# Performance work log

Measured on AMD Instinct MI355X. Metric: run time of the kernel, lower is better.

## Reference

```python
import jax, jax.numpy as jnp
import numpy as np

NTOKEN = 32000
NINP = 512
NHIDLAST = 1024
N_EXPERTS = 10
N = 1024


def setup_inputs() -> dict:
    key = jax.random.key(0)
    ks = jax.random.split(key, 4)
    return {
        "output": jax.random.normal(ks[0], (N, NHIDLAST), dtype=jnp.float32),
        "W_latent": jax.random.normal(ks[1], (N_EXPERTS * NINP, NHIDLAST), dtype=jnp.float32) * 0.02,
        "b_latent": jnp.zeros((N_EXPERTS * NINP,), dtype=jnp.float32),
        "W_decoder": jax.random.normal(ks[2], (NTOKEN, NINP), dtype=jnp.float32) * 0.02,
        "b_decoder": jnp.zeros((NTOKEN,), dtype=jnp.float32),
        "W_reduce": jax.random.normal(ks[3], (N_EXPERTS, NHIDLAST), dtype=jnp.float32) * 0.02,
        "b_reduce": jnp.zeros((N_EXPERTS,), dtype=jnp.float32),
        "dropoutl": 0,
    }


def reference(output, W_latent, b_latent, W_decoder, b_decoder, W_reduce, b_reduce, dropoutl):
    n = output.shape[0]
    # latent projection + tanh; lockdrop with rate 0 is identity
    latent = jnp.tanh(output @ W_latent.T + b_latent)            # [N, E*ninp]
    logit = latent.reshape(n * N_EXPERTS, NINP) @ W_decoder.T + b_decoder  # [N*E, V]
    # stick-breaking Beta parameters
    a = jax.nn.softplus(output @ W_reduce.T + b_reduce) + 1e-8   # [N, E]
    b = jnp.sum(a, axis=1)                                       # [N]
    c = jnp.cumsum(a, axis=1)                                    # [N, E]
    d = jnp.abs(b[:, None] - c)                                  # remaining mass
    d = jnp.maximum(d, 1e-8)  # last column is exactly 0; avoid Beta(a,0) NaN
    sample = jax.random.beta(jax.random.key(42), a, d)           # reparameterized Beta
    # rem @ diag(ones, offset=1) shifts columns right by one; rem[:,0]=1
    rem = 1.0 - sample
    rem_shift = jnp.concatenate([jnp.ones((n, 1), dtype=rem.dtype), rem[:, :-1]], axis=1)
    remprod = jnp.cumprod(rem_shift, axis=1)
    pis = remprod * sample                                       # [N, E] mixture weights
    prob = jax.nn.softmax(logit.reshape(n, N_EXPERTS, NTOKEN), axis=-1)
    out = jnp.einsum('net,ne->nt', prob, pis)                    # [N, V]
    return out
```

## Files before the change

### kernel.cpp

```cpp
#include <hip/hip_runtime.h>
#include <cstdint>
#include <cstddef>

#pragma clang fp contract(off)

#define NTOK  32000
#define NINP  512
#define NHID  1024
#define NEXP  10
#define NROW  1024
#define NLAT  (NEXP*NINP)
#define MROWS (NROW*NEXP)

typedef __attribute__((ext_vector_type(4))) float f32x4;
typedef __attribute__((ext_vector_type(8))) short bf16x8;
typedef __attribute__((ext_vector_type(8))) unsigned short us16x8;

#define GLD16(g, l) __builtin_amdgcn_global_load_lds(                       \
    (const __attribute__((address_space(1))) void*)(g),                     \
    (__attribute__((address_space(3))) void*)(l), 16, 0, 0)

__device__ __forceinline__ unsigned short f2b(float x) {
    uint32_t u = __float_as_uint(x);
    uint32_t r = (u + 0x7fffu + ((u >> 16) & 1u)) >> 16;
    return (unsigned short)r;
}
__device__ __forceinline__ float b2f(unsigned short b) {
    return __uint_as_float(((uint32_t)b) << 16);
}

__device__ __forceinline__ uint32_t rotl32(uint32_t v, int r) {
    return (v << r) | (v >> (32 - r));
}

__device__ __forceinline__ void threefry(uint32_t k0, uint32_t k1,
                                         uint32_t x0, uint32_t x1,
                                         uint32_t& o0, uint32_t& o1) {
    uint32_t k2 = k0 ^ k1 ^ 0x1BD11BDAu;
    x0 += k0; x1 += k1;
#define TF_R(r) { x0 += x1; x1 = rotl32(x1, r); x1 ^= x0; }
    TF_R(13) TF_R(15) TF_R(26) TF_R(6)
    x0 += k1; x1 += k2 + 1u;
    TF_R(17) TF_R(29) TF_R(16) TF_R(24)
    x0 += k2; x1 += k0 + 2u;
    TF_R(13) TF_R(15) TF_R(26) TF_R(6)
    x0 += k0; x1 += k1 + 3u;
    TF_R(17) TF_R(29) TF_R(16) TF_R(24)
    x0 += k1; x1 += k2 + 4u;
    TF_R(13) TF_R(15) TF_R(26) TF_R(6)
    x0 += k2; x1 += k0 + 5u;
#undef TF_R
    o0 = x0; o1 = x1;
}

struct RKey { uint32_t a, b; };

__device__ __forceinline__ RKey kfold(RKey k, uint32_t i) {
    RKey r; threefry(k.a, k.b, 0u, i, r.a, r.b); return r;
}
__device__ __forceinline__ uint32_t kbits(RKey k) {
    uint32_t o0, o1; threefry(k.a, k.b, 0u, 0u, o0, o1); return o0 ^ o1;
}
__device__ __forceinline__ float u01(RKey k) {
    uint32_t b = (kbits(k) >> 9) | 0x3f800000u;
    return __uint_as_float(b) - 1.0f;
}
__device__ __forceinline__ float erfinv_xla(float x) {
    float xx = x * x;
    float w = -log1pf(-xx);
    float p;
    if (w < 5.0f) {
        float ww = w - 2.5f;
        p = 2.81022636e-08f;
        p = p * ww; p = p + 3.43273939e-07f;
        p = p * ww; p = p + -3.5233877e-06f;
        p = p * ww; p = p + -4.39150654e-06f;
        p = p * ww; p = p + 0.00021858087f;
        p = p * ww; p = p + -0.00125372503f;
        p = p * ww; p = p + -0.00417768164f;
        p = p * ww; p = p + 0.246640727f;
        p = p * ww; p = p + 1.50140941f;
    } else {
        float ww = sqrtf(w) - 3.0f;
        p = -0.000200214257f;
        p = p * ww; p = p + 0.000100950558f;
        p = p * ww; p = p + 0.00134934322f;
        p = p * ww; p = p + -0.00367342844f;
        p = p * ww; p = p + 0.00573950773f;
        p = p * ww; p = p + -0.0076224613f;
        p = p * ww; p = p + 0.00943887047f;
        p = p * ww; p = p + 1.00167406f;
        p = p * ww; p = p + 2.83297682f;
    }
    return p * x;
}
__device__ __forceinline__ float norm1(RKey k) {
    const float lo = -0.99999994f;
    float f = u01(k);
    float u = f * 2.0f;
    u = u + lo;
    u = fmaxf(lo, u);
    return 1.41421356f * erfinv_xla(u);
}

__device__ float gamma_log(RKey key, float alpha) {
    const float one_third = 0.33333334f;
    bool boost = (alpha >= 1.0f);
    float alpha_orig = alpha;
    if (!boost) alpha = alpha + 1.0f;
    float d = alpha - one_third;
    float c = one_third / sqrtf(d);

    RKey sub = kfold(key, 1u);
    key      = kfold(key, 0u);
    float log_boost = 0.0f;
    if (!boost) {
        float uB = u01(sub);
        log_boost = log1pf(-uB) * (1.0f / alpha_orig);
    }

    float X = 0.f, V = 1.f, U = 2.f;
    int guard = 0;
    do {
        RKey xk = kfold(key, 1u);
        RKey Uk = kfold(key, 2u);
        key     = kfold(key, 0u);
        float x = 0.f, v = -1.f;
        RKey kin = xk;
        int g2 = 0;
        do {
            RKey sk = kfold(kin, 1u);
            kin     = kfold(kin, 0u);
            x = norm1(sk);
            float cx = x * c;
            v = 1.0f + cx;
        } while (v <= 0.0f && ++g2 < 256);
        X = x * x;
        V = (v * v) * v;
        U = u01(Uk);
        float sq = 1.0f - 0.0331f * (X * X);
        if (U < sq) break;
        float bound = (X * 0.5f) + ((d - d * V) + d * logf(V));
        if (logf(U) < bound) break;
    } while (++guard < 256);

    float ls = logf(d) + logf(V);
    ls = ls + log_boost;
    return ls;
}

__global__ void k_a(const float* __restrict__ out_in,
                    const float* __restrict__ Wred,
                    const float* __restrict__ bred,
                    float* __restrict__ a_arr, float* __restrict__ dpar) {
    int n = blockIdx.x;
    int lane = threadIdx.x;
    __shared__ float zred[NEXP];
    const float* orow = out_in + (size_t)n * NHID;
    for (int e = 0; e < NEXP; ++e) {
        const float* wrow = Wred + (size_t)e * NHID;
        float s = 0.f;
        for (int k = lane; k < NHID; k += 64) s += orow[k] * wrow[k];
        for (int off = 32; off; off >>= 1) s += __shfl_xor(s, off);
        if (lane == 0) zred[e] = s + bred[e];
    }
    __syncthreads();
    if (lane == 0) {
        float a[NEXP];
        float b = 0.f;
        for (int e = 0; e < NEXP; ++e) {
            float z = zred[e];
            a[e] = fmaxf(z, 0.f) + log1pf(expf(-fabsf(z))) + 1e-8f;
        }
        for (int e = 0; e < NEXP; ++e) b += a[e];
        float cs = 0.f;
        for (int e = 0; e < NEXP; ++e) {
            cs += a[e];
            float dd = fmaxf(fabsf(b - cs), 1e-8f);
            a_arr[n * NEXP + e] = a[e];
            dpar [n * NEXP + e] = dd;
        }
    }
}

__global__ void k_sample(const float* __restrict__ a_arr,
                         const float* __restrict__ dpar,
                         float* __restrict__ sample) {
    int i = blockIdx.x * 256 + threadIdx.x;
    if (i >= MROWS) return;
    RKey root{0u, 42u};
    RKey ka = kfold(root, 0u);
    RKey kb = kfold(root, 1u);
    float lga = gamma_log(kfold(ka, (uint32_t)i), a_arr[i]);
    float lgb = gamma_log(kfold(kb, (uint32_t)i), dpar[i]);
    float lm = fmaxf(lga, lgb);
    float ea = expf(lga - lm), eb = expf(lgb - lm);
    sample[i] = ea / (ea + eb);
}

__global__ void k_pis(const float* __restrict__ sample, float* __restrict__ pis) {
    int n = blockIdx.x * blockDim.x + threadIdx.x;
    if (n >= NROW) return;
    float rp = 1.0f;
    for (int e = 0; e < NEXP; ++e) {
        float s = sample[n * NEXP + e];
        pis[n * NEXP + e] = rp * s;
        rp = rp * (1.0f - s);
    }
}

__global__ void k_w(const float* __restrict__ pis, const float* __restrict__ Z,
                    float* __restrict__ w, int r0, int cnt) {
    int i = blockIdx.x * 256 + threadIdx.x;
    if (i >= cnt) return;
    int r = r0 + i;
    w[r] = pis[r] / Z[r];
}

__global__ void k_cvt(const float* __restrict__ src, unsigned short* __restrict__ dst, int n) {
    int i = (blockIdx.x * 256 + threadIdx.x) * 8;
    if (i >= n) return;
    float4 v0 = *(const float4*)(src + i);
    float4 v1 = *(const float4*)(src + i + 4);
    us16x8 o;
    o[0] = f2b(v0.x); o[1] = f2b(v0.y); o[2] = f2b(v0.z); o[3] = f2b(v0.w);
    o[4] = f2b(v1.x); o[5] = f2b(v1.y); o[6] = f2b(v1.z); o[7] = f2b(v1.w);
    *(us16x8*)(dst + i) = o;
}

__device__ __forceinline__ void combine_span(const unsigned short* __restrict__ P,
                                             const float* __restrict__ pis,
                                             const float* __restrict__ Z,
                                             float* __restrict__ out,
                                             int n0, int items, int idx0, int stride) {
    for (int idx = idx0; idx < items; idx += stride) {
        int nl = idx / 4000;
        int c8 = (idx - nl * 4000) * 8;
        int n  = n0 + nl;
        float w[NEXP];
#pragma unroll
        for (int e = 0; e < NEXP; ++e)
            w[e] = pis[n * NEXP + e] / Z[n * NEXP + e];
        float s[8] = {0.f,0.f,0.f,0.f,0.f,0.f,0.f,0.f};
        const unsigned short* Pr = P + (size_t)nl * NEXP * NTOK + c8;
#pragma unroll
        for (int e = 0; e < NEXP; ++e) {
            us16x8 v = __builtin_nontemporal_load((const us16x8*)(Pr + (size_t)e * NTOK));
#pragma unroll
            for (int jj = 0; jj < 8; ++jj)
                s[jj] = s[jj] + w[e] * b2f(v[jj]);
        }
        float* orow = out + (size_t)n * NTOK + c8;
        f32x4 o0 = {s[0], s[1], s[2], s[3]};
        f32x4 o1 = {s[4], s[5], s[6], s[7]};
        __builtin_nontemporal_store(o0, (f32x4*)(orow));
        __builtin_nontemporal_store(o1, (f32x4*)(orow + 4));
    }
}

__global__ __launch_bounds__(256)
void k_fin(const unsigned short* __restrict__ P,
           const float* __restrict__ pis,
           const float* __restrict__ Z,
           float* __restrict__ out, int n0, int items) {
    combine_span(P, pis, Z, out, n0, items,
                 (int)(blockIdx.x * 256u + threadIdx.x),
                 (int)(gridDim.x * 256u));
}

__global__ __launch_bounds__(256)
void k_latm(const unsigned short* __restrict__ A,
            const unsigned short* __restrict__ B,
            const float* __restrict__ bias,
            unsigned short* __restrict__ dst) {
    __shared__ unsigned short Als[2][128 * 64];
    __shared__ unsigned short Bls[2][128 * 64];
    const int tid  = threadIdx.x;
    const int lane = tid & 63, wid = tid >> 6;
    const int wm = wid >> 1, wn = wid & 1;
    const uint32_t l = blockIdx.x;
    const int row0 = (int)(l & 7u) * 128;
    const int col0 = (int)(l >> 3) * 128;
    const int lrow8 = lane >> 3, lslot = lane & 7;

    const unsigned short* pA[4];
    const unsigned short* pB[4];
#pragma unroll
    for (int i = 0; i < 4; ++i) {
        int rA = wid * 32 + i * 8 + lrow8;
        pA[i] = A + (size_t)(row0 + rA) * NHID + ((lslot ^ (rA & 7)) << 3);
        int rB = wid * 32 + i * 8 + lrow8;
        pB[i] = B + (size_t)(col0 + rB) * NHID + ((lslot ^ (rB & 7)) << 3);
    }
    int offA[2][4], offB[2][4];
#pragma unroll
    for (int kh = 0; kh < 2; ++kh)
#pragma unroll
        for (int f = 0; f < 4; ++f) {
            int rA = wm * 64 + f * 16 + (lane & 15);
            offA[kh][f] = rA * 128 + ((((lane >> 4) * 16) + kh * 64) ^ ((rA & 7) << 4));
            int rB = wn * 64 + f * 16 + (lane & 15);
            offB[kh][f] = rB * 128 + ((((lane >> 4) * 16) + kh * 64) ^ ((rB & 7) << 4));
        }

    f32x4 acc[4][4];
#pragma unroll
    for (int mf = 0; mf < 4; ++mf)
#pragma unroll
        for (int nf = 0; nf < 4; ++nf) acc[mf][nf] = (f32x4)0.f;

#pragma unroll
    for (int i = 0; i < 4; ++i) {
        GLD16(pA[i], (char*)&Als[0][0] + (wid * 32 + i * 8) * 128); pA[i] += 64;
        GLD16(pB[i], (char*)&Bls[0][0] + (wid * 32 + i * 8) * 128); pB[i] += 64;
    }
    __syncthreads();

#pragma unroll
    for (int t = 0; t < 16; ++t) {
        const int cur = t & 1, nxt = cur ^ 1;
        if (t < 15) {
#pragma unroll
            for (int i = 0; i < 4; ++i) {
                GLD16(pA[i], (char*)&Als[nxt][0] + (wid * 32 + i * 8) * 128); pA[i] += 64;
                GLD16(pB[i], (char*)&Bls[nxt][0] + (wid * 32 + i * 8) * 128); pB[i] += 64;
            }
        }
        const char* Ab = (const char*)&Als[cur][0];
        const char* Bb = (const char*)&Bls[cur][0];
#pragma unroll
        for (int kh = 0; kh < 2; ++kh) {
            bf16x8 af[4], bfr[4];
#pragma unroll
            for (int f = 0; f < 4; ++f) {
                af[f]  = *(const bf16x8*)(Ab + offA[kh][f]);
                bfr[f] = *(const bf16x8*)(Bb + offB[kh][f]);
            }
#pragma unroll
            for (int mf = 0; mf < 4; ++mf)
#pragma unroll
                for (int nf = 0; nf < 4; ++nf)
                    acc[mf][nf] = __builtin_amdgcn_mfma_f32_16x16x32_bf16(
                        af[mf], bfr[nf], acc[mf][nf], 0, 0, 0);
        }
        __syncthreads();
    }

    const int q = lane >> 4, cl = lane & 15;
#pragma unroll
    for (int mf = 0; mf < 4; ++mf) {
#pragma unroll
        for (int nf = 0; nf < 4; ++nf) {
            int col = col0 + wn * 64 + nf * 16 + cl;
            float bc = bias[col];
#pragma unroll
            for (int j = 0; j < 4; ++j) {
                int r = row0 + wm * 64 + mf * 16 + q * 4 + j;
                dst[(size_t)r * NLAT + col] = f2b(tanhf(acc[mf][nf][j] + bc));
            }
        }
    }
}

template<int MODE>
__global__ __launch_bounds__(256)
void k_dec(const unsigned short* __restrict__ A,
           const unsigned short* __restrict__ B,
           const float* __restrict__ bias,
           const float* __restrict__ wmix,
           float* __restrict__ dst,
           unsigned short* __restrict__ Pst,
           int rb0, int nRB, int nGemm,
           const float* __restrict__ pis,
           const float* __restrict__ Zarr,
           float* __restrict__ outp,
           const unsigned short* __restrict__ Pprev,
           int n0prev, int itemsPrev) {
    if (MODE == 3 && (int)blockIdx.x >= nGemm) {
        const int cb = (int)blockIdx.x - nGemm;
        combine_span(Pprev, pis, Zarr, outp, n0prev, itemsPrev,
                     cb * 256 + (int)threadIdx.x,
                     ((int)gridDim.x - nGemm) * 256);
        return;
    }
    __shared__ unsigned short Als[2][160 * 64];
    __shared__ unsigned short Bls[2][128 * 64];
    const int tid  = threadIdx.x;
    const int lane = tid & 63, wid = tid >> 6;
    const int wm = wid >> 1, wn = wid & 1;
    const uint32_t l = blockIdx.x;
    int by_l, bx;
    if (nRB >= 8) {
        const int per = nRB >> 3;
        const uint32_t jb = l >> 3;
        by_l = (int)(l & 7u) * per + (int)(jb % (uint32_t)per);
        bx   = (int)(jb / (uint32_t)per);
    } else {
        by_l = (int)(l % (uint32_t)nRB);
        bx   = (int)(l / (uint32_t)nRB);
    }
    const int by   = rb0 + by_l;
    const int row0 = by * 160;
    const int rl0  = by_l * 160;
    const int col0 = bx * 128;
    const int lrow8 = lane >> 3, lslot = lane & 7;

    const unsigned short* pA[5];
    const unsigned short* pB[4];
#pragma unroll
    for (int i = 0; i < 5; ++i) {
        int rA = wid * 40 + i * 8 + lrow8;
        pA[i] = A + (size_t)(row0 + rA) * 512 + ((lslot ^ (rA & 7)) << 3);
    }
#pragma unroll
    for (int i = 0; i < 4; ++i) {
        int rB = wid * 32 + i * 8 + lrow8;
        pB[i] = B + (size_t)(col0 + rB) * 512 + ((lslot ^ (rB & 7)) << 3);
    }
    int offA[2][5], offB[2][4];
#pragma unroll
    for (int kh = 0; kh < 2; ++kh) {
#pragma unroll
        for (int mf = 0; mf < 5; ++mf) {
            int r = wm * 80 + mf * 16 + (lane & 15);
            offA[kh][mf] = r * 128 + ((((lane >> 4) * 16) + kh * 64) ^ ((r & 7) << 4));
        }
#pragma unroll
        for (int nf = 0; nf < 4; ++nf) {
            int r = wn * 64 + nf * 16 + (lane & 15);
            offB[kh][nf] = r * 128 + ((((lane >> 4) * 16) + kh * 64) ^ ((r & 7) << 4));
        }
    }

    f32x4 acc[5][4];
#pragma unroll
    for (int mf = 0; mf < 5; ++mf)
#pragma unroll
        for (int nf = 0; nf < 4; ++nf) acc[mf][nf] = (f32x4)0.f;

#pragma unroll
    for (int i = 0; i < 5; ++i) {
        GLD16(pA[i], (char*)&Als[0][0] + (wid * 40 + i * 8) * 128); pA[i] += 64;
    }
#pragma unroll
    for (int i = 0; i < 4; ++i) {
        GLD16(pB[i], (char*)&Bls[0][0] + (wid * 32 + i * 8) * 128); pB[i] += 64;
    }
    __syncthreads();

#pragma unroll
    for (int t = 0; t < 8; ++t) {
        const int cur = t & 1, nxt = cur ^ 1;
        if (t < 7) {
#pragma unroll
            for (int i = 0; i < 5; ++i) {
                GLD16(pA[i], (char*)&Als[nxt][0] + (wid * 40 + i * 8) * 128); pA[i] += 64;
            }
#pragma unroll
            for (int i = 0; i < 4; ++i) {
                GLD16(pB[i], (char*)&Bls[nxt][0] + (wid * 32 + i * 8) * 128); pB[i] += 64;
            }
        }
        const char* Ab = (const char*)&Als[cur][0];
        const char* Bb = (const char*)&Bls[cur][0];
#pragma unroll
        for (int kh = 0; kh < 2; ++kh) {
            bf16x8 af[5], bfr[4];
#pragma unroll
            for (int mf = 0; mf < 5; ++mf)
                af[mf] = *(const bf16x8*)(Ab + offA[kh][mf]);
#pragma unroll
            for (int nf = 0; nf < 4; ++nf)
                bfr[nf] = *(const bf16x8*)(Bb + offB[kh][nf]);
#pragma unroll
            for (int mf = 0; mf < 5; ++mf)
#pragma unroll
                for (int nf = 0; nf < 4; ++nf)
                    acc[mf][nf] = __builtin_amdgcn_mfma_f32_16x16x32_bf16(
                        af[mf], bfr[nf], acc[mf][nf], 0, 0, 0);
        }
        __syncthreads();
    }

    const int q = lane >> 4, cl = lane & 15;
    float bv[4];
#pragma unroll
    for (int nf = 0; nf < 4; ++nf) bv[nf] = bias[col0 + wn * 64 + nf * 16 + cl];

    if (MODE == 1 || MODE == 3) {
#pragma unroll
        for (int mf = 0; mf < 5; ++mf) {
#pragma unroll
            for (int jj = 0; jj < 4; ++jj) {
                const int rr = wm * 80 + mf * 16 + q * 4 + jj;
                float p0 = expf(acc[mf][0][jj] + bv[0]);
                float p1 = expf(acc[mf][1][jj] + bv[1]);
                float p2 = expf(acc[mf][2][jj] + bv[2]);
                float p3 = expf(acc[mf][3][jj] + bv[3]);
                float s = ((p0 + p1) + (p2 + p3));
                s += __shfl_xor(s, 1); s += __shfl_xor(s, 2);
                s += __shfl_xor(s, 4); s += __shfl_xor(s, 8);
                if (cl == 0) atomicAdd(&dst[row0 + rr], s);
                if (MODE == 3) {
                    unsigned short* prow =
                        Pst + (size_t)(rl0 + rr) * NTOK + col0 + wn * 64 + cl;
                    __builtin_nontemporal_store(f2b(p0), prow);
                    __builtin_nontemporal_store(f2b(p1), prow + 16);
                    __builtin_nontemporal_store(f2b(p2), prow + 32);
                    __builtin_nontemporal_store(f2b(p3), prow + 48);
                }
            }
        }
    } else {
        float wv[5][4];
#pragma unroll
        for (int mf = 0; mf < 5; ++mf)
#pragma unroll
            for (int jj = 0; jj < 4; ++jj)
                wv[mf][jj] = wmix[row0 + wm * 80 + mf * 16 + q * 4 + jj];
#pragma unroll
        for (int mf = 0; mf < 5; ++mf)
#pragma unroll
            for (int nf = 0; nf < 4; ++nf)
#pragma unroll
                for (int jj = 0; jj < 4; ++jj)
                    acc[mf][nf][jj] = wv[mf][jj] * expf(acc[mf][nf][jj] + bv[nf]);

        const int tok0 = by * 16 + wm * 8;
#pragma unroll
        for (int t = 0; t < 8; ++t) {
#pragma unroll
            for (int nf = 0; nf < 4; ++nf) {
                float s = 0.f;
#pragma unroll
                for (int i = 0; i < 10; ++i) {
                    const int rl = 10 * t + i;
                    const int mf = rl >> 4, qr = (rl >> 2) & 3, jj = rl & 3;
                    s += (q == qr) ? acc[mf][nf][jj] : 0.f;
                }
                s += __shfl_xor(s, 16);
                s += __shfl_xor(s, 32);
                if (q == 0)
                    dst[(size_t)(tok0 + t) * NTOK + col0 + wn * 64 + nf * 16 + cl] = s;
            }
        }
    }
}

extern "C" void kernel_launch(void* const* d_in, const int* in_sizes, int n_in,
                              void* d_out, int out_size, void* d_ws, size_t ws_size,
                              hipStream_t stream) {
    const float* output    = (const float*)d_in[0];
    const float* W_latent  = (const float*)d_in[1];
    const float* b_latent  = (const float*)d_in[2];
    const float* W_decoder = (const float*)d_in[3];
    const float* b_decoder = (const float*)d_in[4];
    const float* W_reduce  = (const float*)d_in[5];
    const float* b_reduce  = (const float*)d_in[6];
    float* out = (float*)d_out;

    char* wsb = (char*)d_ws;
    unsigned short* latb  = (unsigned short*)wsb;
    unsigned short* wdecb = (unsigned short*)(wsb + 10485760);
    float* a_arr  = (float*)(wsb + 10485760 + 32768000);
    float* dpar   = a_arr  + MROWS;
    float* sample = dpar   + MROWS;
    float* pis    = sample + MROWS;
    float* Z      = pis    + MROWS;
    float* wmix   = Z      + MROWS;
    unsigned short* Pbuf = (unsigned short*)(wmix + MROWS);
    const size_t BASE = 10485760ull + 32768000ull + 6ull * MROWS * 4ull;
    const size_t avail = (ws_size > BASE) ? (ws_size - BASE) : 0;

    int CRd = 0, CRs = 0;
    {
        const int cands[4] = {2560, 1280, 640, 320};
        for (int c = 0; c < 4; ++c)
            if (2ull * (size_t)cands[c] * NTOK * 2ull <= avail) { CRd = cands[c]; break; }
        if (CRd == 0) {
            const int cs[5] = {2560, 1280, 640, 320, 160};
            for (int c = 0; c < 5; ++c)
                if ((size_t)cs[c] * NTOK * 2ull <= avail) { CRs = cs[c]; break; }
        }
    }

    unsigned short* outb  = (unsigned short*)d_out;
    unsigned short* wlatb = (unsigned short*)((char*)d_out + 2097152);

    k_a<<<NROW, 64, 0, stream>>>(output, W_reduce, b_reduce, a_arr, dpar);
    k_sample<<<MROWS / 256, 256, 0, stream>>>(a_arr, dpar, sample);
    k_pis<<<(NROW + 255) / 256, 256, 0, stream>>>(sample, pis);

    k_cvt<<<(NTOK * NINP) / 2048, 256, 0, stream>>>(W_decoder, wdecb, NTOK * NINP);
    k_cvt<<<(NROW * NHID) / 2048, 256, 0, stream>>>(output, outb, NROW * NHID);
    k_cvt<<<(NLAT * NHID) / 2048, 256, 0, stream>>>(W_latent, wlatb, NLAT * NHID);

    k_latm<<<320, 256, 0, stream>>>(outb, wlatb, b_latent, latb);

    (void)hipMemsetAsync(Z, 0, MROWS * sizeof(float), stream);

    if (CRd > 0) {
        const int nRB = CRd / 160, nGemm = nRB * 250, nch = MROWS / CRd;
        const int items = (CRd / 10) * 4000;
        for (int ci = 0; ci < nch; ++ci) {
            unsigned short* Pcur  = Pbuf + (size_t)(ci & 1) * CRd * NTOK;
            unsigned short* Pprev = Pbuf + (size_t)((ci & 1) ^ 1) * CRd * NTOK;
            const int extra = (ci > 0) ? 1000 : 0;
            k_dec<3><<<nGemm + extra, 256, 0, stream>>>(
                latb, wdecb, b_decoder, nullptr, Z, Pcur, ci * nRB, nRB, nGemm,
                pis, Z, out, Pprev, (ci - 1) * (CRd / 10), items);
        }
        unsigned short* Plast = Pbuf + (size_t)((nch - 1) & 1) * CRd * NTOK;
        k_fin<<<items / 256, 256, 0, stream>>>(Plast, pis, Z, out,
                                               (nch - 1) * (CRd / 10), items);
    } else if (CRs > 0) {
        const int nRB = CRs / 160;
        const int items = (CRs / 10) * 4000;
        for (int r0 = 0; r0 < MROWS; r0 += CRs) {
            k_dec<3><<<nRB * 250, 256, 0, stream>>>(
                latb, wdecb, b_decoder, nullptr, Z, Pbuf, r0 / 160, nRB, 1 << 30,
                pis, Z, out, nullptr, 0, 0);
            k_fin<<<items / 256, 256, 0, stream>>>(Pbuf, pis, Z, out, r0 / 10, items);
        }
    } else {
        k_dec<1><<<16000, 256, 0, stream>>>(latb, wdecb, b_decoder, nullptr, Z,
                                            nullptr, 0, 64, 1 << 30,
                                            pis, Z, out, nullptr, 0, 0);
        k_w<<<MROWS / 256, 256, 0, stream>>>(pis, Z, wmix, 0, MROWS);
        k_dec<2><<<16000, 256, 0, stream>>>(latb, wdecb, b_decoder, wmix, out,
                                            nullptr, 0, 64, 1 << 30,
                                            pis, Z, out, nullptr, 0, 0);
    }
    (void)in_sizes; (void)n_in; (void)out_size;
}
```

Measured before the change: 831.5 us.

## Stage softmax probabilities through LDS for coalesced stores; shrink final chunk

In the chunked decoder GEMM, the bf16 exp values are now written into a shared-memory tile first and then stored to global memory as full 16-byte rows. Before, each lane issued scattered 2-byte non-temporal stores. The chunk schedule also splits the tail so the last chunk has only 320 rows, which shortens the non-overlapped final combine pass. The cost is an extra barrier and LDS round-trip per block, and a swizzle change for row-block counts that are not multiples of eight.

New measurement: 881.7 us. 6.0% more time.

```diff
diff --git a/kernel.cpp b/kernel.cpp
--- a/kernel.cpp
+++ b/kernel.cpp
@@ -383,14 +383,15 @@
                      ((int)gridDim.x - nGemm) * 256);
         return;
     }
-    __shared__ unsigned short Als[2][160 * 64];
-    __shared__ unsigned short Bls[2][128 * 64];
+    __shared__ __align__(16) unsigned char lds_raw[73728];
+    unsigned short (*Als)[160 * 64] = (unsigned short (*)[160 * 64])lds_raw;
+    unsigned short (*Bls)[128 * 64] = (unsigned short (*)[128 * 64])(lds_raw + 40960);
     const int tid  = threadIdx.x;
     const int lane = tid & 63, wid = tid >> 6;
     const int wm = wid >> 1, wn = wid & 1;
     const uint32_t l = blockIdx.x;
     int by_l, bx;
-    if (nRB >= 8) {
+    if (nRB >= 8 && (nRB & 7) == 0) {
         const int per = nRB >> 3;
         const uint32_t jb = l >> 3;
         by_l = (int)(l & 7u) * per + (int)(jb % (uint32_t)per);
@@ -487,7 +488,7 @@
 #pragma unroll
     for (int nf = 0; nf < 4; ++nf) bv[nf] = bias[col0 + wn * 64 + nf * 16 + cl];
 
-    if (MODE == 1 || MODE == 3) {
+    if (MODE == 3) {
 #pragma unroll
         for (int mf = 0; mf < 5; ++mf) {
 #pragma unroll
@@ -501,14 +502,36 @@
                 s += __shfl_xor(s, 1); s += __shfl_xor(s, 2);
                 s += __shfl_xor(s, 4); s += __shfl_xor(s, 8);
                 if (cl == 0) atomicAdd(&dst[row0 + rr], s);
-                if (MODE == 3) {
-                    unsigned short* prow =
-                        Pst + (size_t)(rl0 + rr) * NTOK + col0 + wn * 64 + cl;
-                    __builtin_nontemporal_store(f2b(p0), prow);
-                    __builtin_nontemporal_store(f2b(p1), prow + 16);
-                    __builtin_nontemporal_store(f2b(p2), prow + 32);
-                    __builtin_nontemporal_store(f2b(p3), prow + 48);
-                }
+                unsigned short* lrow = (unsigned short*)(lds_raw + rr * 272);
+                lrow[wn * 64 + cl]      = f2b(p0);
+                lrow[wn * 64 + 16 + cl] = f2b(p1);
+                lrow[wn * 64 + 32 + cl] = f2b(p2);
+                lrow[wn * 64 + 48 + cl] = f2b(p3);
+            }
+        }
+        __syncthreads();
+        const int rloc = tid >> 4, c16 = tid & 15;
+#pragma unroll
+        for (int it = 0; it < 10; ++it) {
+            int gr = it * 16 + rloc;
+            us16x8 v = *(const us16x8*)(lds_raw + gr * 272 + c16 * 16);
+            __builtin_nontemporal_store(
+                v, (us16x8*)(Pst + (size_t)(rl0 + gr) * NTOK + col0 + c16 * 8));
+        }
+    } else if (MODE == 1) {
+#pragma unroll
+        for (int mf = 0; mf < 5; ++mf) {
+#pragma unroll
+            for (int jj = 0; jj < 4; ++jj) {
+                const int rr = wm * 80 + mf * 16 + q * 4 + jj;
+                float p0 = expf(acc[mf][0][jj] + bv[0]);
+                float p1 = expf(acc[mf][1][jj] + bv[1]);
+                float p2 = expf(acc[mf][2][jj] + bv[2]);
+                float p3 = expf(acc[mf][3][jj] + bv[3]);
+                float s = ((p0 + p1) + (p2 + p3));
+                s += __shfl_xor(s, 1); s += __shfl_xor(s, 2);
+                s += __shfl_xor(s, 4); s += __shfl_xor(s, 8);
+                if (cl == 0) atomicAdd(&dst[row0 + rr], s);
             }
         }
     } else {
@@ -600,19 +623,30 @@
     (void)hipMemsetAsync(Z, 0, MROWS * sizeof(float), stream);
 
     if (CRd > 0) {
-        const int nRB = CRd / 160, nGemm = nRB * 250, nch = MROWS / CRd;
-        const int items = (CRd / 10) * 4000;
+        int chunks[40]; int nch = 0;
+        {
+            int rem = MROWS;
+            while (rem > CRd) { chunks[nch++] = CRd; rem -= CRd; }
+            if (rem > 320) { chunks[nch++] = rem - 320; chunks[nch++] = 320; }
+            else           { chunks[nch++] = rem; }
+        }
+        int r0 = 0, prevRows = 0, prevR0 = 0;
         for (int ci = 0; ci < nch; ++ci) {
+            const int cr = chunks[ci];
+            const int nRB = cr / 160, nGemm = nRB * 250;
             unsigned short* Pcur  = Pbuf + (size_t)(ci & 1) * CRd * NTOK;
             unsigned short* Pprev = Pbuf + (size_t)((ci & 1) ^ 1) * CRd * NTOK;
             const int extra = (ci > 0) ? 1000 : 0;
+            const int itemsPrev = (prevRows / 10) * 4000;
             k_dec<3><<<nGemm + extra, 256, 0, stream>>>(
-                latb, wdecb, b_decoder, nullptr, Z, Pcur, ci * nRB, nRB, nGemm,
-                pis, Z, out, Pprev, (ci - 1) * (CRd / 10), items);
+                latb, wdecb, b_decoder, nullptr, Z, Pcur, r0 / 160, nRB, nGemm,
+                pis, Z, out, Pprev, prevR0 / 10, itemsPrev);
+            prevR0 = r0; prevRows = cr; r0 += cr;
         }
         unsigned short* Plast = Pbuf + (size_t)((nch - 1) & 1) * CRd * NTOK;
-        k_fin<<<items / 256, 256, 0, stream>>>(Plast, pis, Z, out,
-                                               (nch - 1) * (CRd / 10), items);
+        const int itemsLast = (prevRows / 10) * 4000;
+        k_fin<<<(itemsLast + 255) / 256, 256, 0, stream>>>(Plast, pis, Z, out,
+                                                           prevR0 / 10, itemsLast);
     } else if (CRs > 0) {
         const int nRB = CRs / 160;
         const int items = (CRs / 10) * 4000;
```
